# Kernel tuning notes

Hardware: AMD Instinct MI355X
Metric: run time of the kernel (lower is better)

The kernel has to match this reference:

```python
import jax, jax.numpy as jnp
import numpy as np

NUM_NODES = 50000
NUM_FEATS = 64
NUM_HEADS = 2
NUM_EDGES = 800000


def setup_inputs() -> dict:
    key = jax.random.key(0)
    k1, k2, k3 = jax.random.split(key, 3)
    x = jax.random.normal(k1, (NUM_NODES, NUM_FEATS), dtype=jnp.float32)
    # qk_lin: Linear(num_feats, 2*num_feats*num_heads)
    lim = 1.0 / np.sqrt(NUM_FEATS)
    W_qk = jax.random.uniform(k2, (NUM_FEATS, 2 * NUM_HEADS * NUM_FEATS),
                              dtype=jnp.float32, minval=-lim, maxval=lim)
    b_qk = jnp.zeros((2 * NUM_HEADS * NUM_FEATS,), dtype=jnp.float32)
    edge_index = jax.random.randint(k3, (2, NUM_EDGES), 0, NUM_NODES, dtype=jnp.int32)
    return {"x": x, "W_qk": W_qk, "b_qk": b_qk, "edge_index": edge_index}


def reference(x, W_qk, b_qk, edge_index):
    """Edge-restricted multi-head QK attention with sparse softmax over
    each row's outgoing edges, averaged over heads. Returns per-edge
    attention values [E] (sparse COO values; indices == edge_index)."""
    N, F = x.shape
    H = W_qk.shape[1] // (2 * F)
    # qk: [N, 2*H*F] -> [N, H, 2, F]; q/k split matches einops rearranges
    qk = (x @ W_qk + b_qk).reshape(N, H, 2, F)
    q = qk[:, :, 0, :]  # [N, H, F]
    k = qk[:, :, 1, :]  # [N, H, F]
    row, col = edge_index[0], edge_index[1]
    # per-edge per-head scores: q[row] . k[col]  -> [E, H]
    s = jnp.einsum('ehf,ehf->eh', q[row], k[col])
    # sparse softmax over dim=2 (columns) == segment softmax grouped by row
    m = jax.ops.segment_max(s, row, num_segments=N)      # [N, H]
    ex = jnp.exp(s - m[row])                             # [E, H]
    denom = jax.ops.segment_sum(ex, row, num_segments=N)  # [N, H]
    p = ex / denom[row]                                  # [E, H]
    # torch.sparse.sum over heads / num_heads == mean over heads
    return jnp.mean(p, axis=1)  # [E]
```

## Files before the change

### kernel.cpp

```cpp
#include <hip/hip_runtime.h>
#include <hip/hip_bf16.h>


#define NFEAT 64
#define NCOL  256

__global__ __launch_bounds__(256, 4) void gemm_qk(
    const float* __restrict__ x, const float* __restrict__ W, const float* __restrict__ b,
    __hip_bfloat16* __restrict__ qo, __hip_bfloat16* __restrict__ ko, int N)
{
    __shared__ float xsT[NFEAT][68];
    const int tid = threadIdx.x;
    const int tx  = tid & 63;
    const int wv  = tid >> 6;
    const int row0 = blockIdx.x * 64;

    for (int base = tid * 4; base < 64 * NFEAT; base += 256 * 4) {
        int r = base >> 6, i = base & 63;
        float4 v = make_float4(0.f, 0.f, 0.f, 0.f);
        if (row0 + r < N) v = *(const float4*)&x[(size_t)(row0 + r) * NFEAT + i];
        xsT[i + 0][r] = v.x; xsT[i + 1][r] = v.y; xsT[i + 2][r] = v.z; xsT[i + 3][r] = v.w;
    }
    __syncthreads();

    float acc[16][4];
    const float4 bv = *(const float4*)&b[tx * 4];
#pragma unroll
    for (int r = 0; r < 16; ++r) {
        acc[r][0] = bv.x; acc[r][1] = bv.y; acc[r][2] = bv.z; acc[r][3] = bv.w;
    }

    const float4* Wv = (const float4*)W;
    for (int i = 0; i < NFEAT; ++i) {
        float4 w = Wv[i * 64 + tx];
        float xr[16];
#pragma unroll
        for (int r4 = 0; r4 < 4; ++r4) {
            float4 xv = *(const float4*)&xsT[i][wv * 16 + r4 * 4];
            xr[r4 * 4 + 0] = xv.x; xr[r4 * 4 + 1] = xv.y;
            xr[r4 * 4 + 2] = xv.z; xr[r4 * 4 + 3] = xv.w;
        }
#pragma unroll
        for (int r = 0; r < 16; ++r) {
            acc[r][0] += xr[r] * w.x; acc[r][1] += xr[r] * w.y;
            acc[r][2] += xr[r] * w.z; acc[r][3] += xr[r] * w.w;
        }
    }

    const int c0   = tx * 4;
    const int h    = c0 >> 7;
    const int isk  = (c0 & 127) >> 6;
    const int f0   = c0 & 63;
    __hip_bfloat16* dst = isk ? ko : qo;
    const size_t hoff = (size_t)h * 64 + f0;
#pragma unroll
    for (int r = 0; r < 16; ++r) {
        int node = row0 + wv * 16 + r;
        if (node < N) {
            union { ushort4 u; __hip_bfloat16 h4[4]; } pk;
            pk.h4[0] = __float2bfloat16(acc[r][0]);
            pk.h4[1] = __float2bfloat16(acc[r][1]);
            pk.h4[2] = __float2bfloat16(acc[r][2]);
            pk.h4[3] = __float2bfloat16(acc[r][3]);
            *(ushort4*)&dst[(size_t)node * 128 + hoff] = pk.u;
        }
    }
}

__device__ __forceinline__ float dot_bf16x2(unsigned a, unsigned b) {
    float alo = __uint_as_float(a << 16), ahi = __uint_as_float(a & 0xFFFF0000u);
    float blo = __uint_as_float(b << 16), bhi = __uint_as_float(b & 0xFFFF0000u);
    return alo * blo + ahi * bhi;
}

__global__ __launch_bounds__(256) void edge_scores_exp(
    const __hip_bfloat16* __restrict__ q, const __hip_bfloat16* __restrict__ k,
    const int* __restrict__ ei, float* __restrict__ ex_out,
    float* __restrict__ denom, int E)
{
    const int g    = (int)((blockIdx.x * 256 + threadIdx.x) >> 4);
    const int lane = threadIdx.x & 15;
    if (g >= E) return;

    const int row = ei[g];
    const int col = ei[E + g];

    const uint4* qp = (const uint4*)(q + (size_t)row * 128);
    const uint4* kp = (const uint4*)(k + (size_t)col * 128);
    uint4 qa = qp[lane];
    uint4 ka = kp[lane];

    float p = dot_bf16x2(qa.x, ka.x) + dot_bf16x2(qa.y, ka.y)
            + dot_bf16x2(qa.z, ka.z) + dot_bf16x2(qa.w, ka.w);

    p += __shfl_xor(p, 1);
    p += __shfl_xor(p, 2);
    p += __shfl_xor(p, 4);

    if ((lane & 7) == 0) {
        const int h  = lane >> 3;
        const float e = __expf(p);
        ex_out[(size_t)g * 2 + h] = e;
        atomicAdd(&denom[(size_t)row * 2 + h], e);
    }
}

__global__ __launch_bounds__(256) void edge_out_k(
    const int* __restrict__ ei, const float* __restrict__ ex,
    const float* __restrict__ denom, float* __restrict__ out, int E)
{
    const int e = blockIdx.x * 256 + threadIdx.x;
    if (e >= E) return;
    const int row = ei[e];
    const float2 exv = *(const float2*)&ex[(size_t)e * 2];
    const float2 dv  = *(const float2*)&denom[(size_t)row * 2];
    out[e] = 0.5f * (exv.x / dv.x + exv.y / dv.y);
}

extern "C" void kernel_launch(void* const* d_in, const int* in_sizes, int n_in,
                              void* d_out, int out_size, void* d_ws, size_t ws_size,
                              hipStream_t stream)
{
    const float* x   = (const float*)d_in[0];
    const float* W   = (const float*)d_in[1];
    const float* b   = (const float*)d_in[2];
    const int*   ei  = (const int*)d_in[3];
    float*       out = (float*)d_out;

    const int N = in_sizes[0] / NFEAT;
    const int E = in_sizes[3] / 2;

    char* ws = (char*)d_ws;
    size_t off = 0;
    auto alloc = [&](size_t bytes) { void* p = ws + off; off += (bytes + 255) & ~(size_t)255; return p; };
    __hip_bfloat16* q_ws = (__hip_bfloat16*)alloc((size_t)N * 128 * sizeof(__hip_bfloat16));
    __hip_bfloat16* k_ws = (__hip_bfloat16*)alloc((size_t)N * 128 * sizeof(__hip_bfloat16));
    float*    ex_ws  = (float*)alloc((size_t)E * 2 * sizeof(float));
    float*    den_ws = (float*)alloc((size_t)N * 2 * sizeof(float));
    (void)ws_size;

    hipMemsetAsync(den_ws, 0, (size_t)N * 2 * sizeof(float), stream);

    gemm_qk<<<(N + 63) / 64, 256, 0, stream>>>(x, W, b, q_ws, k_ws, N);
    edge_scores_exp<<<((size_t)E * 16 + 255) / 256, 256, 0, stream>>>(q_ws, k_ws, ei, ex_ws, den_ws, E);
    edge_out_k<<<(E + 255) / 256, 256, 0, stream>>>(ei, ex_ws, den_ws, out, E);
}
```

Baseline: 161.3 us.

## Use bf16 MFMA for QK projection and fold denominator zeroing into GEMM

Replaces the FP32 SIMT projection GEMM with a one-wave-per-32-rows kernel built on 16x16x32 bf16 MFMA. A small prep kernel transposes W and converts it to bf16, and x is converted to bf16 in registers. The hipMemset of the softmax denominator is removed and its zeroing is done inside the GEMM kernel, saving one launch. Inputs are now rounded to bf16 before the matmul, which lowers precision, and the output stores are scalar 2-byte writes with a stride of 128 elements between rows, so they are poorly coalesced.

```diff
diff --git a/kernel.cpp b/kernel.cpp
--- a/kernel.cpp
+++ b/kernel.cpp
@@ -5,64 +5,74 @@
 #define NFEAT 64
 #define NCOL  256
 
-__global__ __launch_bounds__(256, 4) void gemm_qk(
-    const float* __restrict__ x, const float* __restrict__ W, const float* __restrict__ b,
-    __hip_bfloat16* __restrict__ qo, __hip_bfloat16* __restrict__ ko, int N)
+typedef __attribute__((ext_vector_type(8))) short bf16x8;
+typedef __attribute__((ext_vector_type(4))) float f32x4;
+
+__device__ __forceinline__ unsigned short f2bf(float f) {
+    union { __hip_bfloat16 h; unsigned short u; } cv;
+    cv.h = __float2bfloat16(f);
+    return cv.u;
+}
+
+__global__ __launch_bounds__(256) void prep_wt(const float* __restrict__ W,
+                                               unsigned short* __restrict__ Wt) {
+    const int k = blockIdx.x;
+    const int c = threadIdx.x;
+    Wt[(size_t)c * 64 + k] = f2bf(W[(size_t)k * 256 + c]);
+}
+
+__global__ __launch_bounds__(64) void gemm_qk_mfma(
+    const float* __restrict__ x, const unsigned short* __restrict__ Wt,
+    const float* __restrict__ b,
+    unsigned short* __restrict__ qo, unsigned short* __restrict__ ko,
+    float* __restrict__ den, int N)
 {
-    __shared__ float xsT[NFEAT][68];
-    const int tid = threadIdx.x;
-    const int tx  = tid & 63;
-    const int wv  = tid >> 6;
-    const int row0 = blockIdx.x * 64;
+    const int lane = threadIdx.x;
+    const int l15  = lane & 15;
+    const int quad = lane >> 4;
+    const int base = blockIdx.x * 32;
 
-    for (int base = tid * 4; base < 64 * NFEAT; base += 256 * 4) {
-        int r = base >> 6, i = base & 63;
-        float4 v = make_float4(0.f, 0.f, 0.f, 0.f);
-        if (row0 + r < N) v = *(const float4*)&x[(size_t)(row0 + r) * NFEAT + i];
-        xsT[i + 0][r] = v.x; xsT[i + 1][r] = v.y; xsT[i + 2][r] = v.z; xsT[i + 3][r] = v.w;
-    }
-    __syncthreads();
+    const int t = blockIdx.x * 64 + lane;
+    if (t < 2 * N) den[t] = 0.f;
 
-    float acc[16][4];
-    const float4 bv = *(const float4*)&b[tx * 4];
+    bf16x8 afrag[2][2];
 #pragma unroll
-    for (int r = 0; r < 16; ++r) {
-        acc[r][0] = bv.x; acc[r][1] = bv.y; acc[r][2] = bv.z; acc[r][3] = bv.w;
-    }
-
-    const float4* Wv = (const float4*)W;
-    for (int i = 0; i < NFEAT; ++i) {
-        float4 w = Wv[i * 64 + tx];
-        float xr[16];
+    for (int s = 0; s < 2; ++s) {
+        int m = base + s * 16 + l15;
+        if (m >= N) m = N - 1;
+        const float* xp = x + (size_t)m * NFEAT + quad * 8;
 #pragma unroll
-        for (int r4 = 0; r4 < 4; ++r4) {
-            float4 xv = *(const float4*)&xsT[i][wv * 16 + r4 * 4];
-            xr[r4 * 4 + 0] = xv.x; xr[r4 * 4 + 1] = xv.y;
-            xr[r4 * 4 + 2] = xv.z; xr[r4 * 4 + 3] = xv.w;
-        }
-#pragma unroll
-        for (int r = 0; r < 16; ++r) {
-            acc[r][0] += xr[r] * w.x; acc[r][1] += xr[r] * w.y;
-            acc[r][2] += xr[r] * w.z; acc[r][3] += xr[r] * w.w;
+        for (int ks = 0; ks < 2; ++ks) {
+            float4 a0 = *(const float4*)(xp + ks * 32);
+            float4 a1 = *(const float4*)(xp + ks * 32 + 4);
+            bf16x8 f;
+            f[0] = f2bf(a0.x); f[1] = f2bf(a0.y); f[2] = f2bf(a0.z); f[3] = f2bf(a0.w);
+            f[4] = f2bf(a1.x); f[5] = f2bf(a1.y); f[6] = f2bf(a1.z); f[7] = f2bf(a1.w);
+            afrag[s][ks] = f;
         }
     }
 
-    const int c0   = tx * 4;
-    const int h    = c0 >> 7;
-    const int isk  = (c0 & 127) >> 6;
-    const int f0   = c0 & 63;
-    __hip_bfloat16* dst = isk ? ko : qo;
-    const size_t hoff = (size_t)h * 64 + f0;
+#pragma unroll 4
+    for (int ct = 0; ct < 16; ++ct) {
+        const int c = ct * 16 + l15;
+        bf16x8 b0 = *(const bf16x8*)(Wt + (size_t)c * 64 + quad * 8);
+        bf16x8 b1 = *(const bf16x8*)(Wt + (size_t)c * 64 + 32 + quad * 8);
+        const float bias = b[c];
+        const int h   = c >> 7;
+        const int isk = (c >> 6) & 1;
+        const int f0  = c & 63;
+        unsigned short* dst = isk ? ko : qo;
 #pragma unroll
-    for (int r = 0; r < 16; ++r) {
-        int node = row0 + wv * 16 + r;
-        if (node < N) {
-            union { ushort4 u; __hip_bfloat16 h4[4]; } pk;
-            pk.h4[0] = __float2bfloat16(acc[r][0]);
-            pk.h4[1] = __float2bfloat16(acc[r][1]);
-            pk.h4[2] = __float2bfloat16(acc[r][2]);
-            pk.h4[3] = __float2bfloat16(acc[r][3]);
-            *(ushort4*)&dst[(size_t)node * 128 + hoff] = pk.u;
+        for (int s = 0; s < 2; ++s) {
+            f32x4 acc = {0.f, 0.f, 0.f, 0.f};
+            acc = __builtin_amdgcn_mfma_f32_16x16x32_bf16(afrag[s][0], b0, acc, 0, 0, 0);
+            acc = __builtin_amdgcn_mfma_f32_16x16x32_bf16(afrag[s][1], b1, acc, 0, 0, 0);
+#pragma unroll
+            for (int r = 0; r < 4; ++r) {
+                const int m = base + s * 16 + quad * 4 + r;
+                if (m < N)
+                    dst[(size_t)m * 128 + h * 64 + f0] = f2bf(acc[r] + bias);
+            }
         }
     }
 }
@@ -74,7 +84,7 @@
 }
 
 __global__ __launch_bounds__(256) void edge_scores_exp(
-    const __hip_bfloat16* __restrict__ q, const __hip_bfloat16* __restrict__ k,
+    const unsigned short* __restrict__ q, const unsigned short* __restrict__ k,
     const int* __restrict__ ei, float* __restrict__ ex_out,
     float* __restrict__ denom, int E)
 {
@@ -133,15 +143,15 @@
     char* ws = (char*)d_ws;
     size_t off = 0;
     auto alloc = [&](size_t bytes) { void* p = ws + off; off += (bytes + 255) & ~(size_t)255; return p; };
-    __hip_bfloat16* q_ws = (__hip_bfloat16*)alloc((size_t)N * 128 * sizeof(__hip_bfloat16));
-    __hip_bfloat16* k_ws = (__hip_bfloat16*)alloc((size_t)N * 128 * sizeof(__hip_bfloat16));
-    float*    ex_ws  = (float*)alloc((size_t)E * 2 * sizeof(float));
-    float*    den_ws = (float*)alloc((size_t)N * 2 * sizeof(float));
+    unsigned short* q_ws  = (unsigned short*)alloc((size_t)N * 128 * 2);
+    unsigned short* k_ws  = (unsigned short*)alloc((size_t)N * 128 * 2);
+    float*          ex_ws = (float*)alloc((size_t)E * 2 * sizeof(float));
+    float*          den_ws= (float*)alloc((size_t)N * 2 * sizeof(float));
+    unsigned short* wt_ws = (unsigned short*)alloc((size_t)NCOL * NFEAT * 2);
     (void)ws_size;
 
-    hipMemsetAsync(den_ws, 0, (size_t)N * 2 * sizeof(float), stream);
-
-    gemm_qk<<<(N + 63) / 64, 256, 0, stream>>>(x, W, b, q_ws, k_ws, N);
+    prep_wt<<<NFEAT, NCOL, 0, stream>>>(W, wt_ws);
+    gemm_qk_mfma<<<(N + 31) / 32, 64, 0, stream>>>(x, wt_ws, b, q_ws, k_ws, den_ws, N);
     edge_scores_exp<<<((size_t)E * 16 + 255) / 256, 256, 0, stream>>>(q_ws, k_ws, ei, ex_ws, den_ws, E);
     edge_out_k<<<(E + 255) / 256, 256, 0, stream>>>(ei, ex_ws, den_ws, out, E);
 }
```

Result: faster. 155.7 us (-3.5%).
